# Optimization experiments

Hardware: AMD Instinct MI355X
Metric: run time of the kernel (lower is better)

## Reference

```python
import jax, jax.numpy as jnp
import numpy as np

B, S, DIM = 2, 2048, 1024
N_HEAD, HEAD_DIM = 16, 64


def setup_inputs() -> dict:
    key = jax.random.key(0)
    k1, k2, k3, k4 = jax.random.split(key, 4)
    x = jax.random.normal(k1, (B, S, DIM), dtype=jnp.float32)
    # rotary table: cos/sin pairs, shape [S, head_dim//2, 2]
    half = HEAD_DIM // 2
    inv_freq = 1.0 / (10000.0 ** (jnp.arange(0, half, dtype=jnp.float32) / half))
    t = jnp.arange(S, dtype=jnp.float32)
    ang = t[:, None] * inv_freq[None, :]
    freqs_cis = jnp.stack([jnp.cos(ang), jnp.sin(ang)], axis=-1)  # [S, half, 2]
    # causal boolean mask [1,1,S,S] (True = attend)
    mask = jnp.tril(jnp.ones((S, S), dtype=bool))[None, None]
    wqkv = jax.random.normal(k2, (3 * DIM, DIM), dtype=jnp.float32) * (DIM ** -0.5)
    wo = jax.random.normal(k3, (DIM, DIM), dtype=jnp.float32) * (DIM ** -0.5)
    return {"x": x, "freqs_cis": freqs_cis, "mask": mask, "wqkv": wqkv, "wo": wo}


def apply_rotary_emb(x, freqs_cis):
    # x: [B, S, H, D]; freqs_cis: [S, D//2, 2]
    xs = x.reshape(*x.shape[:-1], -1, 2)  # [B,S,H,D//2,2]
    fc = freqs_cis[None, :, None, :, :]  # [1,S,1,D//2,2]
    xr, xi = xs[..., 0], xs[..., 1]
    cr, ci = fc[..., 0], fc[..., 1]
    out = jnp.stack([xr * cr - xi * ci, xi * cr + xr * ci], axis=-1)
    return out.reshape(x.shape)


def reference(x, freqs_cis, mask, wqkv, wo):
    bsz, seqlen, _ = x.shape
    qkv = jnp.einsum('bsd,ed->bse', x, wqkv)  # [B,S,3*dim]
    q, k, v = jnp.split(qkv, 3, axis=-1)
    q = q.reshape(bsz, seqlen, N_HEAD, HEAD_DIM)
    k = k.reshape(bsz, seqlen, N_HEAD, HEAD_DIM)
    v = v.reshape(bsz, seqlen, N_HEAD, HEAD_DIM)
    q = apply_rotary_emb(q, freqs_cis)
    k = apply_rotary_emb(k, freqs_cis)
    scale = HEAD_DIM ** -0.5
    scores = jnp.einsum('bqhd,bkhd->bhqk', q, k) * scale  # [B,H,S,S]
    scores = jnp.where(mask, scores, jnp.finfo(scores.dtype).min)
    attn = jax.nn.softmax(scores, axis=-1)
    y = jnp.einsum('bhqk,bkhd->bqhd', attn, v).reshape(bsz, seqlen, N_HEAD * HEAD_DIM)
    return jnp.einsum('bse,de->bsd', y, wo)
```

## Files before the change

### kernel.cpp

```cpp
#include <hip/hip_runtime.h>
#include <hip/hip_bf16.h>
#include <stdint.h>


typedef __attribute__((ext_vector_type(8))) __bf16 bf16x8;
typedef __attribute__((ext_vector_type(4))) float f32x4;
typedef __attribute__((ext_vector_type(16))) float f32x16;

union B8 { uint4 u; bf16x8 v; unsigned short us[8]; };

static __device__ __forceinline__ float bf2f(unsigned short u) {
  union { unsigned int ui; float f; } x; x.ui = ((unsigned int)u) << 16; return x.f;
}
static __device__ __forceinline__ unsigned short f2bf(float f) {
  union { float f; unsigned int ui; } x; x.f = f;
  unsigned int r = x.ui + 0x7fffu + ((x.ui >> 16) & 1u);
  return (unsigned short)(r >> 16);
}
static __device__ __forceinline__ f32x4 mfma16(bf16x8 a, bf16x8 b, f32x4 c) {
  return __builtin_amdgcn_mfma_f32_16x16x32_bf16(a, b, c, 0, 0, 0);
}
static __device__ __forceinline__ f32x16 mfma32(bf16x8 a, bf16x8 b, f32x16 c) {
  return __builtin_amdgcn_mfma_f32_32x32x16_bf16(a, b, c, 0, 0, 0);
}
#define AS1 __attribute__((address_space(1)))
#define AS3 __attribute__((address_space(3)))
static __device__ __forceinline__ void gload_lds16(const void* g, void* l) {
  __builtin_amdgcn_global_load_lds((const AS1 unsigned int*)g,
                                   (AS3 unsigned int*)l, 16, 0, 0);
}

__global__ __launch_bounds__(256) void cvt_all_kernel(
    const float* __restrict__ x, const float* __restrict__ wqkv,
    const float* __restrict__ wo,
    unsigned short* __restrict__ xb, unsigned short* __restrict__ wqkvb,
    unsigned short* __restrict__ wob) {
  int i = blockIdx.x * 256 + threadIdx.x;
  const float* src; unsigned short* dst; int off;
  if (i < 1048576)       { src = x;    dst = xb;    off = i; }
  else if (i < 1835008)  { src = wqkv; dst = wqkvb; off = i - 1048576; }
  else                   { src = wo;   dst = wob;   off = i - 1835008; }
  float4 f = ((const float4*)src)[off];
  ushort4 u;
  u.x = f2bf(f.x); u.y = f2bf(f.y); u.z = f2bf(f.z); u.w = f2bf(f.w);
  ((ushort4*)dst)[off] = u;
}

__global__ __launch_bounds__(256) void qkv_rope_kernel(
    const unsigned short* __restrict__ xb,
    const unsigned short* __restrict__ wqkvb,
    const float* __restrict__ freqs,
    unsigned short* __restrict__ Q,
    unsigned short* __restrict__ K,
    unsigned short* __restrict__ Vt)
{
  __shared__ __align__(16) unsigned short As[128 * 64];
  __shared__ __align__(16) unsigned short Bs[128 * 64];
  const int t = threadIdx.x;
  const int lane = t & 63, wv = t >> 6;
  const int l31 = lane & 31, lh = lane >> 5;
  const int wm = wv >> 1, wn = wv & 1;
  const int tm = blockIdx.x & 31, tn = blockIdx.x >> 5;
  const int m0 = tm * 128, n0 = tn * 128;

  f32x16 acc[2][2] = {};

  for (int k0 = 0; k0 < 1024; k0 += 64) {
    for (int r = 0; r < 4; ++r) {
      int cid = t + 256 * r;
      int row = cid >> 3, jc = cid & 7;
      int sc = jc ^ (row & 7);
      gload_lds16(xb    + (size_t)(m0 + row) * 1024 + k0 + sc * 8, (char*)As + cid * 16);
      gload_lds16(wqkvb + (size_t)(n0 + row) * 1024 + k0 + sc * 8, (char*)Bs + cid * 16);
    }
    __syncthreads();
    for (int kst = 0; kst < 4; ++kst) {
      const int g = kst * 2 + lh;
      bf16x8 a[2], b[2];
      for (int s2 = 0; s2 < 2; ++s2) {
        int ra = wm * 64 + s2 * 32 + l31;
        a[s2] = *(const bf16x8*)((const char*)As + ra * 128 + (g ^ (ra & 7)) * 16);
        int rb = wn * 64 + s2 * 32 + l31;
        b[s2] = *(const bf16x8*)((const char*)Bs + rb * 128 + (g ^ (rb & 7)) * 16);
      }
      for (int sm = 0; sm < 2; ++sm)
        for (int sn = 0; sn < 2; ++sn)
          acc[sm][sn] = mfma32(a[sm], b[sn], acc[sm][sn]);
    }
    __syncthreads();
  }

  for (int sm = 0; sm < 2; ++sm) {
    for (int sn = 0; sn < 2; ++sn) {
      const int e = n0 + wn * 64 + sn * 32 + l31;
      const int seg = e >> 10;
      const int eh = e & 1023;
      const int h = eh >> 6, d = eh & 63;
      for (int r = 0; r < 16; ++r) {
        const int m = m0 + wm * 64 + sm * 32 + (r & 3) + 8 * (r >> 2) + 4 * lh;
        const int b_ = m >> 11, s_ = m & 2047;
        float v = acc[sm][sn][r];
        if (seg == 2) {
          Vt[((size_t)(b_ * 16 + h) * 64 + d) * 2048 + s_] = f2bf(v);
        } else {
          float partner = __shfl_xor(v, 1, 64);
          float cr = freqs[s_ * 64 + (d & ~1)];
          float ci = freqs[s_ * 64 + (d | 1)];
          float outv = (d & 1) ? (v * cr + partner * ci) : (v * cr - partner * ci);
          unsigned short* dst = (seg == 0) ? Q : K;
          dst[((size_t)(b_ * 16 + h) * 2048 + s_) * 64 + d] = f2bf(outv);
        }
      }
    }
  }
}

struct QState {
  bf16x8 qf0, qf1;
  f32x4 o[4];
  float lp[4];
};

static __device__ __forceinline__ void load_q(QState& st,
    const unsigned short* Qb, int q0, int c, int quad) {
  st.qf0 = *(const bf16x8*)(Qb + (q0 + c) * 64 + quad * 8);
  st.qf1 = *(const bf16x8*)(Qb + (q0 + c) * 64 + 32 + quad * 8);
}

static __device__ __forceinline__ void attn_chunk(
    QState& st, const char* Ks, const char* Vs, unsigned short* myp,
    int c, int quad, int k0, int q0, bool diag)
{
  f32x4 sfr[4];
  for (int kc = 0; kc < 4; ++kc) {
    const int key = kc * 16 + c;
    const int s0 = quad ^ (key & 7), s1 = (4 + quad) ^ (key & 7);
    f32x4 sacc = {};
    sacc = mfma16(st.qf0, *(const bf16x8*)(Ks + key * 128 + s0 * 16), sacc);
    sacc = mfma16(st.qf1, *(const bf16x8*)(Ks + key * 128 + s1 * 16), sacc);
    sfr[kc] = sacc;
  }
  for (int i = 0; i < 4; ++i) {
    const int qrow = q0 + quad * 4 + i;
    float e[4];
    for (int kc = 0; kc < 4; ++kc) {
      float arg = fmaf(sfr[kc][i], 0.18033688f, -20.19773057f);
      if (diag && (k0 + kc * 16 + c > qrow)) arg = -1e30f;
      e[kc] = exp2f(arg);
    }
    st.lp[i] += (e[0] + e[1]) + (e[2] + e[3]);
    unsigned short* prow = myp + (quad * 4 + i) * 72;
    prow[c]      = f2bf(e[0]);
    prow[16 + c] = f2bf(e[1]);
    prow[32 + c] = f2bf(e[2]);
    prow[48 + c] = f2bf(e[3]);
  }
  bf16x8 pf[2];
  pf[0] = *(const bf16x8*)(myp + c * 72 + quad * 8);
  pf[1] = *(const bf16x8*)(myp + c * 72 + 32 + quad * 8);
  for (int ct = 0; ct < 4; ++ct) {
    const int d = ct * 16 + c;
    const int s0 = quad ^ (d & 7), s1 = (4 + quad) ^ (d & 7);
    st.o[ct] = mfma16(pf[0], *(const bf16x8*)(Vs + d * 128 + s0 * 16), st.o[ct]);
    st.o[ct] = mfma16(pf[1], *(const bf16x8*)(Vs + d * 128 + s1 * 16), st.o[ct]);
  }
}

__global__ __launch_bounds__(256) void attn_partial_kernel(
    const unsigned short* __restrict__ Q,
    const unsigned short* __restrict__ K,
    const unsigned short* __restrict__ Vt,
    unsigned short* __restrict__ Po,
    float* __restrict__ Pl)
{
  __shared__ __align__(16) unsigned short Ks[64 * 64];
  __shared__ __align__(16) unsigned short Vs[64 * 64];
  __shared__ __align__(16) unsigned short plds[4][16 * 72];
  const int t = threadIdx.x;
  const int lane = t & 63, wv = t >> 6;
  const int c = lane & 15, quad = lane >> 4;
  const int bh = blockIdx.x & 31;
  const int rest = blockIdx.x >> 5;
  const int j = rest >> 1, half = rest & 1;
  const int qA = j * 64 + wv * 16;
  const int qB = (31 - j) * 64 + wv * 16;

  const unsigned short* Qb = Q + (size_t)bh * (2048 * 64);
  const unsigned short* Kb = K + (size_t)bh * (2048 * 64);
  const unsigned short* Vb = Vt + (size_t)bh * (64 * 2048);

  QState A = {}, Bst = {};
  load_q(A, Qb, qA, c, quad);
  load_q(Bst, Qb, qB, c, quad);

  unsigned short* myp = plds[wv];
  const int ktmax = 31 - j;

  for (int kt = half; kt <= ktmax; kt += 2) {
    const int k0 = kt * 64;
    __syncthreads();
    for (int r = 0; r < 2; ++r) {
      int cid = t + 256 * r;
      int row = cid >> 3, jc = cid & 7;
      int sc = jc ^ (row & 7);
      gload_lds16(Kb + (size_t)(k0 + row) * 64 + sc * 8, (char*)Ks + cid * 16);
      gload_lds16(Vb + (size_t)row * 2048 + k0 + sc * 8, (char*)Vs + cid * 16);
    }
    __syncthreads();
    attn_chunk(Bst, (const char*)Ks, (const char*)Vs, myp, c, quad,
               k0, qB, kt == ktmax);
    if (kt <= j)
      attn_chunk(A, (const char*)Ks, (const char*)Vs, myp, c, quad,
                 k0, qA, kt == j);
  }

  unsigned short* Poh = Po + (size_t)half * (32 * 2048 * 64) + (size_t)bh * (2048 * 64);
  float* Plh = Pl + (size_t)half * (32 * 2048) + bh * 2048;
  for (int set = 0; set < 2; ++set) {
    QState& st = set ? Bst : A;
    const int q0 = set ? qB : qA;
    for (int i = 0; i < 4; ++i) {
      float l = st.lp[i];
      l += __shfl_xor(l, 1, 16);
      l += __shfl_xor(l, 2, 16);
      l += __shfl_xor(l, 4, 16);
      l += __shfl_xor(l, 8, 16);
      const int s = q0 + quad * 4 + i;
      for (int ct = 0; ct < 4; ++ct)
        Poh[(size_t)s * 64 + ct * 16 + c] = f2bf(st.o[ct][i]);
      if (c == 0) Plh[s] = l;
    }
  }
}

__global__ __launch_bounds__(256) void combine_kernel(
    const unsigned short* __restrict__ Po, const float* __restrict__ Pl,
    unsigned short* __restrict__ Yb)
{
  const int idx = blockIdx.x * 256 + threadIdx.x;
  const int bh = idx >> 14, rem = idx & 16383;
  const int s = rem >> 3, g = rem & 7;
  const size_t base = (size_t)bh * (2048 * 64) + (size_t)s * 64 + g * 8;
  B8 a, b;
  a.u = *(const uint4*)(Po + base);
  b.u = *(const uint4*)(Po + (size_t)(32 * 2048 * 64) + base);
  float l = Pl[bh * 2048 + s] + Pl[32 * 2048 + bh * 2048 + s];
  float inv = 1.0f / l;
  B8 y;
  for (int k = 0; k < 8; ++k)
    y.us[k] = f2bf((bf2f(a.us[k]) + bf2f(b.us[k])) * inv);
  const int b_ = bh >> 4, h = bh & 15;
  *(uint4*)(Yb + ((size_t)(b_ * 2048 + s)) * 1024 + h * 64 + g * 8) = y.u;
}

__global__ __launch_bounds__(256) void attn_kernel(
    const unsigned short* __restrict__ Q,
    const unsigned short* __restrict__ K,
    const unsigned short* __restrict__ Vt,
    unsigned short* __restrict__ Y)
{
  __shared__ __align__(16) unsigned short Ks[64 * 64];
  __shared__ __align__(16) unsigned short Vs[64 * 64];
  __shared__ __align__(16) unsigned short plds[4][16 * 72];
  const int t = threadIdx.x;
  const int lane = t & 63, wv = t >> 6;
  const int c = lane & 15, quad = lane >> 4;
  const int j = blockIdx.x >> 5, bh = blockIdx.x & 31;
  const int b = bh >> 4, h = bh & 15;
  const int qA = j * 64 + wv * 16;
  const int qB = (31 - j) * 64 + wv * 16;

  const unsigned short* Qb = Q + (size_t)bh * (2048 * 64);
  const unsigned short* Kb = K + (size_t)bh * (2048 * 64);
  const unsigned short* Vb = Vt + (size_t)bh * (64 * 2048);

  QState A = {}, Bst = {};
  load_q(A, Qb, qA, c, quad);
  load_q(Bst, Qb, qB, c, quad);

  const int nkt = 32 - j;
  unsigned short* myp = plds[wv];

  for (int kt = 0; kt < nkt; ++kt) {
    const int k0 = kt * 64;
    __syncthreads();
    for (int r = 0; r < 2; ++r) {
      int cid = t + 256 * r;
      int row = cid >> 3, jc = cid & 7;
      int sc = jc ^ (row & 7);
      gload_lds16(Kb + (size_t)(k0 + row) * 64 + sc * 8, (char*)Ks + cid * 16);
      gload_lds16(Vb + (size_t)row * 2048 + k0 + sc * 8, (char*)Vs + cid * 16);
    }
    __syncthreads();
    attn_chunk(Bst, (const char*)Ks, (const char*)Vs, myp, c, quad,
               k0, qB, kt == 31 - j);
    if (kt <= j)
      attn_chunk(A, (const char*)Ks, (const char*)Vs, myp, c, quad,
                 k0, qA, kt == j);
  }

  for (int set = 0; set < 2; ++set) {
    QState& st = set ? Bst : A;
    const int q0 = set ? qB : qA;
    for (int i = 0; i < 4; ++i) {
      float l = st.lp[i];
      l += __shfl_xor(l, 1, 16);
      l += __shfl_xor(l, 2, 16);
      l += __shfl_xor(l, 4, 16);
      l += __shfl_xor(l, 8, 16);
      float inv = 1.0f / l;
      const int s = q0 + quad * 4 + i;
      unsigned short* dst = Y + ((size_t)(b * 2048 + s)) * 1024 + h * 64;
      for (int ct = 0; ct < 4; ++ct)
        dst[ct * 16 + c] = f2bf(st.o[ct][i] * inv);
    }
  }
}

__global__ __launch_bounds__(256) void out_proj_kernel(
    const unsigned short* __restrict__ Y,
    const unsigned short* __restrict__ wob,
    float* __restrict__ out)
{
  __shared__ __align__(16) unsigned short As[64 * 64];
  __shared__ __align__(16) unsigned short Bs[64 * 64];
  const int t = threadIdx.x;
  const int lane = t & 63, wv = t >> 6;
  const int c = lane & 15, quad = lane >> 4;
  const int wm = wv >> 1, wn = wv & 1;
  const int tm = blockIdx.x & 63, tn = blockIdx.x >> 6;
  const int m0 = tm * 64, n0 = tn * 64;

  f32x4 acc[2][2] = {};

  for (int k0 = 0; k0 < 1024; k0 += 64) {
    for (int r = 0; r < 2; ++r) {
      int cid = t + 256 * r;
      int row = cid >> 3, jc = cid & 7;
      int sc = jc ^ (row & 7);
      gload_lds16(Y   + (size_t)(m0 + row) * 1024 + k0 + sc * 8, (char*)As + cid * 16);
      gload_lds16(wob + (size_t)(n0 + row) * 1024 + k0 + sc * 8, (char*)Bs + cid * 16);
    }
    __syncthreads();
    for (int ks = 0; ks < 2; ++ks) {
      bf16x8 a[2], b[2];
      for (int st = 0; st < 2; ++st) {
        int ra = wm * 32 + st * 16 + c;
        int sa = (ks * 4 + quad) ^ (ra & 7);
        a[st] = *(const bf16x8*)((const char*)As + ra * 128 + sa * 16);
        int rb = wn * 32 + st * 16 + c;
        int sb = (ks * 4 + quad) ^ (rb & 7);
        b[st] = *(const bf16x8*)((const char*)Bs + rb * 128 + sb * 16);
      }
      for (int sm = 0; sm < 2; ++sm)
        for (int sn = 0; sn < 2; ++sn)
          acc[sm][sn] = mfma16(a[sm], b[sn], acc[sm][sn]);
    }
    __syncthreads();
  }

  for (int sm = 0; sm < 2; ++sm)
    for (int sn = 0; sn < 2; ++sn)
      for (int i = 0; i < 4; ++i) {
        const int m = m0 + wm * 32 + sm * 16 + quad * 4 + i;
        const int e = n0 + wn * 32 + sn * 16 + c;
        out[(size_t)m * 1024 + e] = acc[sm][sn][i];
      }
}

extern "C" void kernel_launch(void* const* d_in, const int* in_sizes, int n_in,
                              void* d_out, int out_size, void* d_ws, size_t ws_size,
                              hipStream_t stream) {
  const float* x     = (const float*)d_in[0];
  const float* freqs = (const float*)d_in[1];
  const float* wqkv  = (const float*)d_in[3];
  const float* wo    = (const float*)d_in[4];
  float* out = (float*)d_out;

  const size_t BHSD = (size_t)2 * 16 * 2048 * 64;
  unsigned short* Q     = (unsigned short*)d_ws;
  unsigned short* K     = Q + BHSD;
  unsigned short* Vt    = K + BHSD;
  unsigned short* Yb    = Vt + BHSD;
  unsigned short* xb    = Yb + BHSD;
  unsigned short* wqkvb = xb + 4194304;
  unsigned short* wob   = wqkvb + 3145728;
  unsigned short* Po    = wob + 1048576;
  float*          Pl    = (float*)(Po + 2 * BHSD);

  const size_t need_fast =
      (size_t)((char*)(Pl + 2 * 32 * 2048) - (char*)d_ws);

  cvt_all_kernel<<<8192, 256, 0, stream>>>(x, wqkv, wo, xb, wqkvb, wob);
  qkv_rope_kernel<<<768, 256, 0, stream>>>(xb, wqkvb, freqs, Q, K, Vt);
  if (ws_size >= need_fast) {
    attn_partial_kernel<<<1024, 256, 0, stream>>>(Q, K, Vt, Po, Pl);
    combine_kernel<<<2048, 256, 0, stream>>>(Po, Pl, Yb);
  } else {
    attn_kernel<<<512, 256, 0, stream>>>(Q, K, Vt, Yb);
  }
  out_proj_kernel<<<1024, 256, 0, stream>>>(Yb, wob, out);
}
```

Before: 220.2 us.

## Retile out-projection to 128x64 with 32x32 MFMA, vectorize rope and bf16 packing

The output projection moves from 64x64 tiles using 16x16x32 MFMAs to 128x64 tiles using 32x32x16 MFMAs, halving the grid and increasing operand reuse per LDS load. The rotary cos/sin pair is now fetched with a single float2 load, and the softmax probabilities are converted to bf16 with the hardware packed-convert instruction in place of manual rounding. The larger tile uses more LDS and registers, and the halved grid may lower occupancy or leave CUs underfilled.

```diff
diff --git a/kernel.cpp b/kernel.cpp
--- a/kernel.cpp
+++ b/kernel.cpp
@@ -16,6 +16,11 @@
   union { float f; unsigned int ui; } x; x.f = f;
   unsigned int r = x.ui + 0x7fffu + ((x.ui >> 16) & 1u);
   return (unsigned short)(r >> 16);
+}
+static __device__ __forceinline__ unsigned int cvt_pk_bf16(float lo, float hi) {
+  unsigned int r;
+  asm("v_cvt_pk_bf16_f32 %0, %1, %2" : "=v"(r) : "v"(lo), "v"(hi));
+  return r;
 }
 static __device__ __forceinline__ f32x4 mfma16(bf16x8 a, bf16x8 b, f32x4 c) {
   return __builtin_amdgcn_mfma_f32_16x16x32_bf16(a, b, c, 0, 0, 0);
@@ -104,9 +109,9 @@
           Vt[((size_t)(b_ * 16 + h) * 64 + d) * 2048 + s_] = f2bf(v);
         } else {
           float partner = __shfl_xor(v, 1, 64);
-          float cr = freqs[s_ * 64 + (d & ~1)];
-          float ci = freqs[s_ * 64 + (d | 1)];
-          float outv = (d & 1) ? (v * cr + partner * ci) : (v * cr - partner * ci);
+          float2 fc = *(const float2*)(freqs + s_ * 64 + (d & ~1));
+          float outv = (d & 1) ? (v * fc.x + partner * fc.y)
+                               : (v * fc.x - partner * fc.y);
           unsigned short* dst = (seg == 0) ? Q : K;
           dst[((size_t)(b_ * 16 + h) * 2048 + s_) * 64 + d] = f2bf(outv);
         }
@@ -149,11 +154,13 @@
       e[kc] = exp2f(arg);
     }
     st.lp[i] += (e[0] + e[1]) + (e[2] + e[3]);
+    unsigned int u01 = cvt_pk_bf16(e[0], e[1]);
+    unsigned int u23 = cvt_pk_bf16(e[2], e[3]);
     unsigned short* prow = myp + (quad * 4 + i) * 72;
-    prow[c]      = f2bf(e[0]);
-    prow[16 + c] = f2bf(e[1]);
-    prow[32 + c] = f2bf(e[2]);
-    prow[48 + c] = f2bf(e[3]);
+    prow[c]      = (unsigned short)u01;
+    prow[16 + c] = (unsigned short)(u01 >> 16);
+    prow[32 + c] = (unsigned short)u23;
+    prow[48 + c] = (unsigned short)(u23 >> 16);
   }
   bf16x8 pf[2];
   pf[0] = *(const bf16x8*)(myp + c * 72 + quad * 8);
@@ -322,50 +329,52 @@
     const unsigned short* __restrict__ wob,
     float* __restrict__ out)
 {
-  __shared__ __align__(16) unsigned short As[64 * 64];
+  __shared__ __align__(16) unsigned short As[128 * 64];
   __shared__ __align__(16) unsigned short Bs[64 * 64];
   const int t = threadIdx.x;
   const int lane = t & 63, wv = t >> 6;
-  const int c = lane & 15, quad = lane >> 4;
+  const int l31 = lane & 31, lh = lane >> 5;
   const int wm = wv >> 1, wn = wv & 1;
-  const int tm = blockIdx.x & 63, tn = blockIdx.x >> 6;
-  const int m0 = tm * 64, n0 = tn * 64;
-
-  f32x4 acc[2][2] = {};
+  const int tm = blockIdx.x & 31, tn = blockIdx.x >> 5;
+  const int m0 = tm * 128, n0 = tn * 64;
+
+  f32x16 acc[2] = {};
 
   for (int k0 = 0; k0 < 1024; k0 += 64) {
+    for (int r = 0; r < 4; ++r) {
+      int cid = t + 256 * r;
+      int row = cid >> 3, jc = cid & 7;
+      int sc = jc ^ (row & 7);
+      gload_lds16(Y + (size_t)(m0 + row) * 1024 + k0 + sc * 8, (char*)As + cid * 16);
+    }
     for (int r = 0; r < 2; ++r) {
       int cid = t + 256 * r;
       int row = cid >> 3, jc = cid & 7;
       int sc = jc ^ (row & 7);
-      gload_lds16(Y   + (size_t)(m0 + row) * 1024 + k0 + sc * 8, (char*)As + cid * 16);
       gload_lds16(wob + (size_t)(n0 + row) * 1024 + k0 + sc * 8, (char*)Bs + cid * 16);
     }
     __syncthreads();
-    for (int ks = 0; ks < 2; ++ks) {
-      bf16x8 a[2], b[2];
-      for (int st = 0; st < 2; ++st) {
-        int ra = wm * 32 + st * 16 + c;
-        int sa = (ks * 4 + quad) ^ (ra & 7);
-        a[st] = *(const bf16x8*)((const char*)As + ra * 128 + sa * 16);
-        int rb = wn * 32 + st * 16 + c;
-        int sb = (ks * 4 + quad) ^ (rb & 7);
-        b[st] = *(const bf16x8*)((const char*)Bs + rb * 128 + sb * 16);
+    for (int kst = 0; kst < 4; ++kst) {
+      const int g = kst * 2 + lh;
+      bf16x8 a[2], b;
+      for (int s2 = 0; s2 < 2; ++s2) {
+        int ra = wm * 64 + s2 * 32 + l31;
+        a[s2] = *(const bf16x8*)((const char*)As + ra * 128 + (g ^ (ra & 7)) * 16);
       }
-      for (int sm = 0; sm < 2; ++sm)
-        for (int sn = 0; sn < 2; ++sn)
-          acc[sm][sn] = mfma16(a[sm], b[sn], acc[sm][sn]);
-    }
-    __syncthreads();
-  }
-
+      int rb = wn * 32 + l31;
+      b = *(const bf16x8*)((const char*)Bs + rb * 128 + (g ^ (rb & 7)) * 16);
+      acc[0] = mfma32(a[0], b, acc[0]);
+      acc[1] = mfma32(a[1], b, acc[1]);
+    }
+    __syncthreads();
+  }
+
+  const int col = n0 + wn * 32 + l31;
   for (int sm = 0; sm < 2; ++sm)
-    for (int sn = 0; sn < 2; ++sn)
-      for (int i = 0; i < 4; ++i) {
-        const int m = m0 + wm * 32 + sm * 16 + quad * 4 + i;
-        const int e = n0 + wn * 32 + sn * 16 + c;
-        out[(size_t)m * 1024 + e] = acc[sm][sn][i];
-      }
+    for (int r = 0; r < 16; ++r) {
+      const int m = m0 + wm * 64 + sm * 32 + (r & 3) + 8 * (r >> 2) + 4 * lh;
+      out[(size_t)m * 1024 + col] = acc[sm][r];
+    }
 }
 
 extern "C" void kernel_launch(void* const* d_in, const int* in_sizes, int n_in,
@@ -399,5 +408,5 @@
   } else {
     attn_kernel<<<512, 256, 0, stream>>>(Q, K, Vt, Yb);
   }
-  out_proj_kernel<<<1024, 256, 0, stream>>>(Yb, wob, out);
-}
+  out_proj_kernel<<<512, 256, 0, stream>>>(Yb, wob, out);
+}
```

New measurement: 210.1 us. -4.6%, faster.
